# Kernel tuning notes

Hardware: AMD Instinct MI355X
Metric: run time of the kernel (lower is better)

## Reference

```python
import jax, jax.numpy as jnp
import numpy as np

B, C, T = 8, 1024, 4096
H, K = 16, 15          # n_heads, kernel_size
PAD = K // 2           # 'same' padding so output length == T


def setup_inputs() -> dict:
    key = jax.random.key(0)
    k1, k2 = jax.random.split(key)
    x = jax.random.normal(k1, (B, C, T), dtype=jnp.float32)
    # weight_linear: Linear(C -> H*K, bias=False); scaled small for sane softmax
    W_lin = jax.random.normal(k2, (H * K, C), dtype=jnp.float32) * 0.02
    return {"x": x, "W_lin": W_lin}


def reference(x, W_lin):
    """Dynamic lightweight conv: per-(b,t) softmax kernels applied depthwise.
    x: (B, C, T) -> (B, C, T). Channel c uses head c % H (matches view(-1,H,T)).
    """
    Bb, Cc, Tt = x.shape
    R = Cc // H
    # kernel generation: (B,T,H,K), softmax over taps K
    proj = jnp.einsum('bct,fc->btf', x, W_lin).reshape(Bb, Tt, H, K)
    w = jax.nn.softmax(proj, axis=-1)
    w = jnp.transpose(w, (0, 2, 3, 1))            # (B, H, K, T)
    # group channels by head: c = r*H + h  ->  head h = c % H
    xr = x.reshape(Bb, R, H, Tt)                  # (B, R, H, T)
    xpad = jnp.pad(xr, ((0, 0), (0, 0), (0, 0), (PAD, PAD)))
    out = jnp.zeros_like(xr)
    for k in range(K):  # small fixed tap count; avoids (B,C,T,K) unfold blowup
        out = out + w[:, None, :, k, :] * xpad[..., k:k + Tt]
    return out.reshape(Bb, Cc, Tt)
```

## Files before the change

### kernel.cpp

```cpp
#include <hip/hip_runtime.h>
#include <hip/hip_bf16.h>

constexpr int Bn  = 8;
constexpr int Cn  = 1024;
constexpr int Tn  = 4096;
constexpr int Hn  = 16;
constexpr int Kn  = 15;
constexpr int Fp  = 256;

typedef __attribute__((ext_vector_type(8))) short    bf16x8;
typedef __attribute__((ext_vector_type(4))) float    f32x4;

static __device__ __forceinline__ unsigned short f2bf(float f) {
    __hip_bfloat16 h = __float2bfloat16(f);
    return *reinterpret_cast<unsigned short*>(&h);
}

__global__ __launch_bounds__(256)
void lwc_wpad(const float* __restrict__ W, unsigned short* __restrict__ Wp)
{
    const int idx = (blockIdx.x * 256 + threadIdx.x) * 4;
    const int m = idx >> 10, c = idx & 1023;
    const int h = m >> 4, k = m & 15;
    float4 v = make_float4(0.f, 0.f, 0.f, 0.f);
    if (k < 15)
        v = *reinterpret_cast<const float4*>(W + ((size_t)(h * 15 + k)) * Cn + c);
    ushort4 o;
    o.x = f2bf(v.x); o.y = f2bf(v.y); o.z = f2bf(v.z); o.w = f2bf(v.w);
    *reinterpret_cast<ushort4*>(Wp + idx) = o;
}

__global__ __launch_bounds__(256)
void lwc_fused_weights(const float* __restrict__ x,
                       const unsigned short* __restrict__ Wp,
                       float* __restrict__ wout)
{
    __shared__ __align__(16) unsigned short xs[2 * 16 * 64 * 8];

    const int tid  = threadIdx.x;
    const int lane = tid & 63;
    const int wv   = tid >> 6;
    const int t0   = blockIdx.x * 64;
    const int b    = blockIdx.y;

    const int lr = lane & 15;
    const int lg = lane >> 4;

    const int tcell = tid & 15;
    const int coct  = tid >> 4;
    const float* xbase = x + (size_t)b * Cn * Tn + t0 + tcell * 4;

    f32x4 acc[4][4];
#pragma unroll
    for (int i = 0; i < 4; ++i)
#pragma unroll
        for (int j = 0; j < 4; ++j) acc[i][j] = (f32x4){0.f, 0.f, 0.f, 0.f};

    float4 ld[8];
#pragma unroll
    for (int j = 0; j < 8; ++j)
        ld[j] = *reinterpret_cast<const float4*>(
            xbase + (size_t)(coct * 8 + j) * Tn);

    const unsigned short* Abase = Wp + ((size_t)(wv * 64 + lr)) * Cn + lg * 8;
    const int lrx0 = lr ^ lg;
    unsigned short* wrow = xs + coct * 512;
    const int csw = coct & 7;

#pragma unroll 1
    for (int ck = 0; ck < 8; ++ck) {
        const int buf = (ck & 1) * 8192;

        float cf[8][4];
#pragma unroll
        for (int j = 0; j < 8; ++j) {
            cf[j][0] = ld[j].x; cf[j][1] = ld[j].y;
            cf[j][2] = ld[j].z; cf[j][3] = ld[j].w;
        }
#pragma unroll
        for (int tt = 0; tt < 4; ++tt) {
            const int slotw = (tcell * 4 + tt) ^ csw;
            bf16x8 pk;
#pragma unroll
            for (int j = 0; j < 8; ++j) pk[j] = (short)f2bf(cf[j][tt]);
            *reinterpret_cast<bf16x8*>(wrow + buf + slotw * 8) = pk;
        }

        __syncthreads();

        if (ck < 7) {
#pragma unroll
            for (int j = 0; j < 8; ++j)
                ld[j] = *reinterpret_cast<const float4*>(
                    xbase + (size_t)((ck + 1) * 128 + coct * 8 + j) * Tn);
        }

        const unsigned short* Apc = Abase + ck * 128;
#pragma unroll
        for (int ks = 0; ks < 4; ++ks) {
            bf16x8 af[4], bfr[4];
            const unsigned short* ap = Apc + ks * 32;
#pragma unroll
            for (int mi = 0; mi < 4; ++mi)
                af[mi] = *reinterpret_cast<const bf16x8*>(ap + (size_t)mi * 16 * Cn);
            const int lrx = lrx0 ^ ((ks & 1) << 2);
            const unsigned short* bp = xs + buf + (ks * 4 + lg) * 512 + lrx * 8;
#pragma unroll
            for (int ni = 0; ni < 4; ++ni)
                bfr[ni] = *reinterpret_cast<const bf16x8*>(bp + ni * 128);
#pragma unroll
            for (int mi = 0; mi < 4; ++mi)
#pragma unroll
                for (int ni = 0; ni < 4; ++ni)
                    acc[mi][ni] = __builtin_amdgcn_mfma_f32_16x16x32_bf16(
                        af[mi], bfr[ni], acc[mi][ni], 0, 0, 0);
        }
    }

    const int tcol = lane & 15;
#pragma unroll
    for (int mi = 0; mi < 4; ++mi) {
        const int h = wv * 4 + mi;
        float* hbase = wout + (((size_t)b * Hn + h) * Kn) * Tn + t0;
#pragma unroll
        for (int ni = 0; ni < 4; ++ni) {
            f32x4 v = acc[mi][ni];
            float mx = -3.0e38f;
#pragma unroll
            for (int r = 0; r < 4; ++r)
                if (lg * 4 + r < 15) mx = fmaxf(mx, v[r]);
            mx = fmaxf(mx, __shfl_xor(mx, 16));
            mx = fmaxf(mx, __shfl_xor(mx, 32));
            float e[4], s = 0.f;
#pragma unroll
            for (int r = 0; r < 4; ++r) {
                const int k = lg * 4 + r;
                e[r] = (k < 15) ? __expf(v[r] - mx) : 0.f;
                s += e[r];
            }
            s += __shfl_xor(s, 16);
            s += __shfl_xor(s, 32);
            const float inv = 1.f / s;
#pragma unroll
            for (int r = 0; r < 4; ++r) {
                const int k = lg * 4 + r;
                if (k < 15)
                    hbase[(size_t)k * Tn + ni * 16 + tcol] = e[r] * inv;
            }
        }
    }
}

__global__ __launch_bounds__(256)
void lwc_apply(const float* __restrict__ x,
               const float* __restrict__ w,
               float* __restrict__ out)
{
    const int tid  = threadIdx.x;
    const int tq   = tid & 15;
    const int cgrp = tid >> 4;
    const int t0   = blockIdx.x * 64;
    const int h    = blockIdx.y;
    const int b    = blockIdx.z;

    const int tb = t0 + tq * 4;

    const float* wb = w + (((size_t)b * Hn + h) * Kn) * Tn + tb;
    float4 wreg[15];
#pragma unroll
    for (int k = 0; k < 15; ++k)
        wreg[k] = *reinterpret_cast<const float4*>(wb + (size_t)k * Tn);

    const int g0 = tb - 8;
    const bool interior = (g0 >= 0) && (g0 + 20 <= Tn);
    const float* xb = x + (size_t)b * Cn * Tn;
    float*       ob = out + (size_t)b * Cn * Tn;

#pragma unroll
    for (int j = 0; j < 4; ++j) {
        const int c = (cgrp * 4 + j) * Hn + h;
        const float* xrow = xb + (size_t)c * Tn;

        float xv[20];
        if (interior) {
            const float4* xp = reinterpret_cast<const float4*>(xrow + g0);
#pragma unroll
            for (int q = 0; q < 5; ++q) {
                const float4 a = xp[q];
                xv[4 * q + 0] = a.x; xv[4 * q + 1] = a.y;
                xv[4 * q + 2] = a.z; xv[4 * q + 3] = a.w;
            }
        } else {
#pragma unroll
            for (int i = 0; i < 20; ++i) {
                const int g = g0 + i;
                xv[i] = ((unsigned)g < (unsigned)Tn) ? xrow[g] : 0.f;
            }
        }

        float ox = 0.f, oy = 0.f, oz = 0.f, ow = 0.f;
#pragma unroll
        for (int k = 0; k < 15; ++k) {
            ox += wreg[k].x * xv[k + 1];
            oy += wreg[k].y * xv[k + 2];
            oz += wreg[k].z * xv[k + 3];
            ow += wreg[k].w * xv[k + 4];
        }
        f32x4 o = {ox, oy, oz, ow};
        __builtin_nontemporal_store(
            o, reinterpret_cast<f32x4*>(ob + (size_t)c * Tn + tb));
    }
}

extern "C" void kernel_launch(void* const* d_in, const int* in_sizes, int n_in,
                              void* d_out, int out_size, void* d_ws, size_t ws_size,
                              hipStream_t stream)
{
    const float* x = (const float*)d_in[0];
    const float* W = (const float*)d_in[1];
    float* out     = (float*)d_out;
    float* wks     = (float*)d_ws;

    unsigned short* Wp = (unsigned short*)d_out;

    lwc_wpad<<<dim3(Fp * Cn / 4 / 256), 256, 0, stream>>>(W, Wp);

    dim3 gF(Tn / 64, Bn);
    lwc_fused_weights<<<gF, 256, 0, stream>>>(x, Wp, wks);

    dim3 gB(Tn / 64, Hn, Bn);
    lwc_apply<<<gB, 256, 0, stream>>>(x, wks, out);
}
```

Baseline: 131.1 us.

## Store softmax weights in bf16 and widen apply tile to eight outputs per thread

The softmax conv weights written to the workspace are now stored as bf16 instead of fp32, which halves the intermediate write and read traffic. The apply kernel now has each thread compute 8 consecutive outputs instead of 4, so grid blocks cover 128 time steps. This reduces redundant halo loads of x and makes better use of each load, at the cost of more registers per thread. The weights lose precision through bf16 rounding, but they are softmax values in [0,1], so the error should be small.

```diff
diff --git a/kernel.cpp b/kernel.cpp
--- a/kernel.cpp
+++ b/kernel.cpp
@@ -33,7 +33,7 @@
 __global__ __launch_bounds__(256)
 void lwc_fused_weights(const float* __restrict__ x,
                        const unsigned short* __restrict__ Wp,
-                       float* __restrict__ wout)
+                       unsigned short* __restrict__ wout)
 {
     __shared__ __align__(16) unsigned short xs[2 * 16 * 64 * 8];
 
@@ -121,7 +121,7 @@
 #pragma unroll
     for (int mi = 0; mi < 4; ++mi) {
         const int h = wv * 4 + mi;
-        float* hbase = wout + (((size_t)b * Hn + h) * Kn) * Tn + t0;
+        unsigned short* hbase = wout + (((size_t)b * Hn + h) * Kn) * Tn + t0;
 #pragma unroll
         for (int ni = 0; ni < 4; ++ni) {
             f32x4 v = acc[mi][ni];
@@ -145,7 +145,7 @@
             for (int r = 0; r < 4; ++r) {
                 const int k = lg * 4 + r;
                 if (k < 15)
-                    hbase[(size_t)k * Tn + ni * 16 + tcol] = e[r] * inv;
+                    hbase[(size_t)k * Tn + ni * 16 + tcol] = f2bf(e[r] * inv);
             }
         }
     }
@@ -153,26 +153,25 @@
 
 __global__ __launch_bounds__(256)
 void lwc_apply(const float* __restrict__ x,
-               const float* __restrict__ w,
+               const unsigned short* __restrict__ w,
                float* __restrict__ out)
 {
     const int tid  = threadIdx.x;
     const int tq   = tid & 15;
     const int cgrp = tid >> 4;
-    const int t0   = blockIdx.x * 64;
+    const int t0   = blockIdx.x * 128;
     const int h    = blockIdx.y;
     const int b    = blockIdx.z;
-
-    const int tb = t0 + tq * 4;
-
-    const float* wb = w + (((size_t)b * Hn + h) * Kn) * Tn + tb;
-    float4 wreg[15];
+    const int tb   = t0 + tq * 8;
+
+    const unsigned short* wb = w + (((size_t)b * Hn + h) * Kn) * Tn + tb;
+    bf16x8 wk[15];
 #pragma unroll
     for (int k = 0; k < 15; ++k)
-        wreg[k] = *reinterpret_cast<const float4*>(wb + (size_t)k * Tn);
+        wk[k] = *reinterpret_cast<const bf16x8*>(wb + (size_t)k * Tn);
 
     const int g0 = tb - 8;
-    const bool interior = (g0 >= 0) && (g0 + 20 <= Tn);
+    const bool interior = (g0 >= 0) && (g0 + 24 <= Tn);
     const float* xb = x + (size_t)b * Cn * Tn;
     float*       ob = out + (size_t)b * Cn * Tn;
 
@@ -181,34 +180,39 @@
         const int c = (cgrp * 4 + j) * Hn + h;
         const float* xrow = xb + (size_t)c * Tn;
 
-        float xv[20];
+        float xv[24];
         if (interior) {
             const float4* xp = reinterpret_cast<const float4*>(xrow + g0);
 #pragma unroll
-            for (int q = 0; q < 5; ++q) {
+            for (int q = 0; q < 6; ++q) {
                 const float4 a = xp[q];
                 xv[4 * q + 0] = a.x; xv[4 * q + 1] = a.y;
                 xv[4 * q + 2] = a.z; xv[4 * q + 3] = a.w;
             }
         } else {
 #pragma unroll
-            for (int i = 0; i < 20; ++i) {
+            for (int i = 0; i < 24; ++i) {
                 const int g = g0 + i;
                 xv[i] = ((unsigned)g < (unsigned)Tn) ? xrow[g] : 0.f;
             }
         }
 
-        float ox = 0.f, oy = 0.f, oz = 0.f, ow = 0.f;
+        float o8[8] = {0.f, 0.f, 0.f, 0.f, 0.f, 0.f, 0.f, 0.f};
 #pragma unroll
         for (int k = 0; k < 15; ++k) {
-            ox += wreg[k].x * xv[k + 1];
-            oy += wreg[k].y * xv[k + 2];
-            oz += wreg[k].z * xv[k + 3];
-            ow += wreg[k].w * xv[k + 4];
-        }
-        f32x4 o = {ox, oy, oz, ow};
-        __builtin_nontemporal_store(
-            o, reinterpret_cast<f32x4*>(ob + (size_t)c * Tn + tb));
+#pragma unroll
+            for (int jj = 0; jj < 8; ++jj) {
+                const unsigned int u =
+                    ((unsigned int)(unsigned short)wk[k][jj]) << 16;
+                o8[jj] += __uint_as_float(u) * xv[jj + k + 1];
+            }
+        }
+
+        f32x4 o0 = {o8[0], o8[1], o8[2], o8[3]};
+        f32x4 o1 = {o8[4], o8[5], o8[6], o8[7]};
+        float* dst = ob + (size_t)c * Tn + tb;
+        __builtin_nontemporal_store(o0, reinterpret_cast<f32x4*>(dst));
+        __builtin_nontemporal_store(o1, reinterpret_cast<f32x4*>(dst + 4));
     }
 }
 
@@ -219,7 +223,7 @@
     const float* x = (const float*)d_in[0];
     const float* W = (const float*)d_in[1];
     float* out     = (float*)d_out;
-    float* wks     = (float*)d_ws;
+    unsigned short* wks = (unsigned short*)d_ws;
 
     unsigned short* Wp = (unsigned short*)d_out;
 
@@ -228,6 +232,6 @@
     dim3 gF(Tn / 64, Bn);
     lwc_fused_weights<<<gF, 256, 0, stream>>>(x, Wp, wks);
 
-    dim3 gB(Tn / 64, Hn, Bn);
+    dim3 gB(Tn / 128, Hn, Bn);
     lwc_apply<<<gB, 256, 0, stream>>>(x, wks, out);
 }
```

New measurement: 120.6 us. -8.0%, faster.
